# Kernel optimization log

Measured on AMD Instinct MI355X. Metric: run time of the kernel, lower is better.

Reference implementation:

```python
import jax, jax.numpy as jnp
import numpy as np

N_NODES = 100_000
N_EDGES = 1_600_000
IN_DIM = 512
HID = 128
OUT_DIM = 40


def setup_inputs() -> dict:
    key = jax.random.key(0)
    ks = jax.random.split(key, 12)
    s = 0.05  # small init scale
    x = jax.random.normal(ks[0], (N_NODES, IN_DIM), dtype=jnp.float32)
    edge_index = jax.random.randint(ks[1], (2, N_EDGES), 0, N_NODES, dtype=jnp.int64)
    W1 = jax.random.normal(ks[2], (IN_DIM, HID), dtype=jnp.float32) * s
    b1 = jnp.zeros((HID,), jnp.float32)
    Wg0 = jax.random.normal(ks[3], (HID, HID), dtype=jnp.float32) * s
    bg0 = jnp.zeros((HID,), jnp.float32)
    Wg1 = jax.random.normal(ks[4], (HID, HID), dtype=jnp.float32) * s
    bg1 = jnp.zeros((HID,), jnp.float32)
    W2 = jax.random.normal(ks[5], (HID, OUT_DIM), dtype=jnp.float32) * s
    b2 = jnp.zeros((OUT_DIM,), jnp.float32)
    return dict(x=x, edge_index=edge_index, W1=W1, b1=b1, Wg0=Wg0, bg0=bg0,
                Wg1=Wg1, bg1=bg1, W2=W2, b2=b2)


def _gcn_norm(edge_index, num_nodes, dtype):
    # PyG GCNConv default: add self-loops, symmetric normalization D^-1/2 A D^-1/2.
    loops = jnp.arange(num_nodes, dtype=edge_index.dtype)
    src = jnp.concatenate([edge_index[0], loops])  # [E+N]
    dst = jnp.concatenate([edge_index[1], loops])
    deg = jax.ops.segment_sum(jnp.ones(dst.shape, dtype), dst, num_segments=num_nodes)
    dinv = jnp.where(deg > 0, jax.lax.rsqrt(deg), jnp.zeros((), dtype))
    norm = dinv[src] * dinv[dst]  # [E+N]
    return src, dst, norm


def _gcn_conv(h, src, dst, norm, W, b, num_nodes):
    # out[dst] += norm * (h @ W)[src]; then bias
    hw = h @ W                              # [N, HID]
    msg = hw[src] * norm[:, None]           # gather + scale  [E+N, HID]
    agg = jax.ops.segment_sum(msg, dst, num_segments=num_nodes)  # scatter-add
    return agg + b


def reference(x, edge_index, W1, b1, Wg0, bg0, Wg1, bg1, W2, b2):
    n = x.shape[0]
    src, dst, norm = _gcn_norm(edge_index, n, x.dtype)
    h = jax.nn.relu(x @ W1 + b1)  # dropout is identity in eval mode
    for W, b in ((Wg0, bg0), (Wg1, bg1)):
        h = jax.nn.relu(_gcn_conv(h, src, dst, norm, W, b, n))
    logits = h @ W2 + b2
    return jax.nn.log_softmax(logits, axis=1)
```

## Files before the change

### kernel.cpp

```cpp
#include <hip/hip_runtime.h>
#include <hip/hip_bf16.h>
#include <cstdint>

#define HID 128

typedef short s16x8 __attribute__((ext_vector_type(8)));
typedef float f32x4 __attribute__((ext_vector_type(4)));

static inline size_t align_up(size_t x, size_t a) { return (x + a - 1) & ~(a - 1); }

__device__ inline ushort f2bf(float f) {
  uint u = __float_as_uint(f);
  u += 0x7FFFu + ((u >> 16) & 1u);
  return (ushort)(u >> 16);
}
__device__ inline float bf2f_lo(uint v) { return __uint_as_float(v << 16); }
__device__ inline float bf2f_hi(uint v) { return __uint_as_float(v & 0xFFFF0000u); }

__global__ void detect_i64_kernel(const unsigned int* __restrict__ p, int nwords,
                                  int* __restrict__ flag) {
  __shared__ int any;
  if (threadIdx.x == 0) any = 0;
  __syncthreads();
  for (int i = threadIdx.x; i < 1024; i += blockDim.x) {
    int w = 2 * i + 1;
    if (w < nwords && p[w] != 0u) atomicOr(&any, 1);
  }
  __syncthreads();
  if (threadIdx.x == 0) *flag = (any == 0) ? 1 : 0;
}

__global__ void extract_kernel(const void* __restrict__ ei, const int* __restrict__ flag,
                               int E, int* __restrict__ src32, int* __restrict__ dst32) {
  int e = blockIdx.x * blockDim.x + threadIdx.x;
  if (e >= E) return;
  if (*flag) {
    const long long* p = (const long long*)ei;
    src32[e] = (int)p[e];
    dst32[e] = (int)p[(size_t)E + e];
  } else {
    const int* p = (const int*)ei;
    src32[e] = p[e];
    dst32[e] = p[(size_t)E + e];
  }
}

__global__ void count_kernel(const int* __restrict__ dst32, int* __restrict__ cnt, int E) {
  int e = blockIdx.x * blockDim.x + threadIdx.x;
  if (e >= E) return;
  atomicAdd(&cnt[dst32[e]], 1);
}

__global__ void dinv_kernel(const int* __restrict__ cnt, float* __restrict__ dinv, int N) {
  int i = blockIdx.x * blockDim.x + threadIdx.x;
  if (i >= N) return;
  dinv[i] = rsqrtf((float)(cnt[i] + 1));
}

__global__ __launch_bounds__(1024) void scan_local_kernel(const int* __restrict__ cnt,
    int* __restrict__ off, int* __restrict__ bsum, int N) {
  __shared__ int buf[1024];
  int tid = threadIdx.x;
  int i = blockIdx.x * 1024 + tid;
  int v = (i < N) ? cnt[i] : 0;
  buf[tid] = v;
  __syncthreads();
  #pragma unroll
  for (int s = 1; s < 1024; s <<= 1) {
    int t = (tid >= s) ? buf[tid - s] : 0;
    __syncthreads();
    buf[tid] += t;
    __syncthreads();
  }
  if (i < N) off[i] = buf[tid] - v;
  if (tid == 1023) bsum[blockIdx.x] = buf[1023];
}

__global__ __launch_bounds__(128) void scan_bsum_kernel(const int* __restrict__ bsum, int nb,
    int* __restrict__ boff, int* __restrict__ offN) {
  __shared__ int b[128];
  int tid = threadIdx.x;
  int v = (tid < nb) ? bsum[tid] : 0;
  b[tid] = v;
  __syncthreads();
  #pragma unroll
  for (int s = 1; s < 128; s <<= 1) {
    int t = (tid >= s) ? b[tid - s] : 0;
    __syncthreads();
    b[tid] += t;
    __syncthreads();
  }
  if (tid < nb) boff[tid] = b[tid] - v;
  if (tid == 127) *offN = b[127];
}

__global__ void scan_add_kernel(int* __restrict__ off, const int* __restrict__ boff,
                                int* __restrict__ cursor, int N) {
  int i = blockIdx.x * blockDim.x + threadIdx.x;
  if (i >= N) return;
  int o = off[i] + boff[i >> 10];
  off[i] = o;
  cursor[i] = o;
}

__global__ void fill_kernel(const int* __restrict__ src32, const int* __restrict__ dst32,
                            const float* __restrict__ dinv, int* __restrict__ cursor,
                            int* __restrict__ csr_src, float* __restrict__ csr_norm, int E) {
  int e = blockIdx.x * blockDim.x + threadIdx.x;
  if (e >= E) return;
  int s = src32[e];
  int d = dst32[e];
  int pos = atomicAdd(&cursor[d], 1);
  csr_src[pos] = s;
  csr_norm[pos] = dinv[s] * dinv[d];
}

__global__ void convert_w_kernel(const float* __restrict__ W, ushort* __restrict__ Wt,
                                 int K, int KP) {
  int id = blockIdx.x * blockDim.x + threadIdx.x;
  if (id >= K * 128) return;
  int c = id & 127;
  int k = id >> 7;
  Wt[(size_t)c * KP + k] = f2bf(W[id]);
}

__global__ void convert_w2_kernel(const float* __restrict__ W2, ushort* __restrict__ Wt) {
  int id = blockIdx.x * blockDim.x + threadIdx.x;
  if (id >= 48 * 128) return;
  int c = id >> 7;
  int k = id & 127;
  Wt[(size_t)c * 128 + k] = (c < 40) ? f2bf(W2[(size_t)k * 40 + c]) : (ushort)0;
}

template <int K, bool AF32, bool BIAS_RELU, int WAVES>
__global__ __launch_bounds__(WAVES * 64, 16 / WAVES) void gemm_lds_kernel(
    const void* __restrict__ Ap, const ushort* __restrict__ Wtp,
    const float* __restrict__ bias, ushort* __restrict__ outp,
    int M, int rowsPerBlock) {
  constexpr int KP = K + 8;
  extern __shared__ __align__(16) ushort lB[];
  const int tid = threadIdx.x;

  const int rowStart = blockIdx.x * rowsPerBlock;
  if (rowStart >= M) return;
  const int rowEnd = min(M, rowStart + rowsPerBlock);

  constexpr int TOTC = 128 * KP / 8;
  const s16x8* Wt8 = (const s16x8*)Wtp;
  for (int i = tid; i < TOTC; i += WAVES * 64) ((s16x8*)lB)[i] = Wt8[i];
  __syncthreads();

  const int w = tid >> 6;
  const int l = tid & 63;
  const int l15 = l & 15;
  const int kg = l >> 4;

  const ushort* Ab = (const ushort*)Ap;
  const float* Af = (const float*)Ap;

  for (int base = rowStart + w * 16; base < rowEnd; base += WAVES * 16) {
    int row = base + l15;
    if (row >= M) row = M - 1;

    f32x4 acc[8];
    #pragma unroll
    for (int c = 0; c < 8; ++c) acc[c] = f32x4{0.f, 0.f, 0.f, 0.f};

    #pragma unroll 4
    for (int k0 = 0; k0 < K; k0 += 32) {
      s16x8 af;
      if constexpr (AF32) {
        const float* s = &Af[(size_t)row * K + k0 + kg * 8];
        float4 v0 = *(const float4*)s;
        float4 v1 = *(const float4*)(s + 4);
        af[0] = (short)f2bf(v0.x); af[1] = (short)f2bf(v0.y);
        af[2] = (short)f2bf(v0.z); af[3] = (short)f2bf(v0.w);
        af[4] = (short)f2bf(v1.x); af[5] = (short)f2bf(v1.y);
        af[6] = (short)f2bf(v1.z); af[7] = (short)f2bf(v1.w);
      } else {
        af = *(const s16x8*)&Ab[(size_t)row * K + k0 + kg * 8];
      }
      #pragma unroll
      for (int c = 0; c < 8; ++c) {
        s16x8 bfr = *(const s16x8*)&lB[(16 * c + l15) * KP + k0 + kg * 8];
        acc[c] = __builtin_amdgcn_mfma_f32_16x16x32_bf16(af, bfr, acc[c], 0, 0, 0);
      }
    }

    #pragma unroll
    for (int c = 0; c < 8; ++c) {
      float b = 0.f;
      if constexpr (BIAS_RELU) b = bias[16 * c + l15];
      #pragma unroll
      for (int v = 0; v < 4; ++v) {
        int r = base + kg * 4 + v;
        if (r < M) {
          float val = acc[c][v];
          if constexpr (BIAS_RELU) val = fmaxf(val + b, 0.f);
          outp[(size_t)r * 128 + 16 * c + l15] = f2bf(val);
        }
      }
    }
  }
}

__global__ __launch_bounds__(256) void aggregate_bf16_kernel(const ushort* __restrict__ hw,
    const int* __restrict__ off, const int* __restrict__ csr_src,
    const float* __restrict__ csr_norm, const float* __restrict__ dinv,
    const float* __restrict__ bias, ushort* __restrict__ out, int N) {
  int wid = (blockIdx.x * blockDim.x + threadIdx.x) >> 6;
  int lane = threadIdx.x & 63;
  if (wid >= N) return;
  const uint* hw4 = (const uint*)hw;
  int beg = off[wid], end = off[wid + 1];
  float ax = 0.f, ay = 0.f;
  int j = beg;
  for (; j + 4 <= end; j += 4) {
    int s0 = csr_src[j];
    int s1 = csr_src[j + 1];
    int s2 = csr_src[j + 2];
    int s3 = csr_src[j + 3];
    float n0 = csr_norm[j];
    float n1 = csr_norm[j + 1];
    float n2 = csr_norm[j + 2];
    float n3 = csr_norm[j + 3];
    uint v0 = hw4[(size_t)s0 * 64 + lane];
    uint v1 = hw4[(size_t)s1 * 64 + lane];
    uint v2 = hw4[(size_t)s2 * 64 + lane];
    uint v3 = hw4[(size_t)s3 * 64 + lane];
    ax = fmaf(n0, bf2f_lo(v0), ax); ay = fmaf(n0, bf2f_hi(v0), ay);
    ax = fmaf(n1, bf2f_lo(v1), ax); ay = fmaf(n1, bf2f_hi(v1), ay);
    ax = fmaf(n2, bf2f_lo(v2), ax); ay = fmaf(n2, bf2f_hi(v2), ay);
    ax = fmaf(n3, bf2f_lo(v3), ax); ay = fmaf(n3, bf2f_hi(v3), ay);
  }
  for (; j < end; ++j) {
    int s = csr_src[j];
    float nm = csr_norm[j];
    uint v = hw4[(size_t)s * 64 + lane];
    ax = fmaf(nm, bf2f_lo(v), ax);
    ay = fmaf(nm, bf2f_hi(v), ay);
  }
  float di = dinv[wid];
  float snm = di * di;
  uint v = hw4[(size_t)wid * 64 + lane];
  ax = fmaf(snm, bf2f_lo(v), ax);
  ay = fmaf(snm, bf2f_hi(v), ay);
  float2 b = ((const float2*)bias)[lane];
  float ox = fmaxf(ax + b.x, 0.f);
  float oy = fmaxf(ay + b.y, 0.f);
  ((uint*)out)[(size_t)wid * 64 + lane] = (uint)f2bf(ox) | ((uint)f2bf(oy) << 16);
}

__global__ __launch_bounds__(256) void final_mfma_kernel(const ushort* __restrict__ h,
    const ushort* __restrict__ W2t, const float* __restrict__ b2,
    float* __restrict__ out, int M) {
  const int tid = threadIdx.x;
  const int w = tid >> 6;
  const int l = tid & 63;
  const int l15 = l & 15;
  const int kg = l >> 4;
  const int base = (blockIdx.x * 4 + w) * 16;
  if (base >= M) return;
  int row = base + l15;
  if (row >= M) row = M - 1;

  f32x4 acc[3];
  #pragma unroll
  for (int c = 0; c < 3; ++c) acc[c] = f32x4{0.f, 0.f, 0.f, 0.f};

  #pragma unroll
  for (int k0 = 0; k0 < 128; k0 += 32) {
    s16x8 af = *(const s16x8*)&h[(size_t)row * 128 + k0 + kg * 8];
    #pragma unroll
    for (int c = 0; c < 3; ++c) {
      s16x8 bfr = *(const s16x8*)&W2t[(size_t)(16 * c + l15) * 128 + k0 + kg * 8];
      acc[c] = __builtin_amdgcn_mfma_f32_16x16x32_bf16(af, bfr, acc[c], 0, 0, 0);
    }
  }

  float bv0 = b2[l15];
  float bv1 = b2[16 + l15];
  float bv2 = (l15 < 8) ? b2[32 + l15] : 0.f;

  #pragma unroll
  for (int v = 0; v < 4; ++v) {
    float l0 = acc[0][v] + bv0;
    float l1 = acc[1][v] + bv1;
    float l2 = (l15 < 8) ? (acc[2][v] + bv2) : -1e30f;
    float pm = fmaxf(fmaxf(l0, l1), l2);
    #pragma unroll
    for (int sh = 8; sh > 0; sh >>= 1) pm = fmaxf(pm, __shfl_xor(pm, sh));
    float es = expf(l0 - pm) + expf(l1 - pm) + ((l15 < 8) ? expf(l2 - pm) : 0.f);
    #pragma unroll
    for (int sh = 8; sh > 0; sh >>= 1) es += __shfl_xor(es, sh);
    float lse = pm + logf(es);
    int r = base + kg * 4 + v;
    if (r < M) {
      out[(size_t)r * 40 + l15] = l0 - lse;
      out[(size_t)r * 40 + 16 + l15] = l1 - lse;
      if (l15 < 8) out[(size_t)r * 40 + 32 + l15] = l2 - lse;
    }
  }
}

extern "C" void kernel_launch(void* const* d_in, const int* in_sizes, int n_in,
                              void* d_out, int out_size, void* d_ws, size_t ws_size,
                              hipStream_t stream) {
  const float* x   = (const float*)d_in[0];
  const void*  ei  = d_in[1];
  const float* W1  = (const float*)d_in[2];
  const float* b1  = (const float*)d_in[3];
  const float* Wg0 = (const float*)d_in[4];
  const float* bg0 = (const float*)d_in[5];
  const float* Wg1 = (const float*)d_in[6];
  const float* bg1 = (const float*)d_in[7];
  const float* W2  = (const float*)d_in[8];
  const float* b2  = (const float*)d_in[9];
  float* out = (float*)d_out;

  const int N = in_sizes[0] / 512;
  const int E = in_sizes[1] / 2;

  char* wsb = (char*)d_ws;
  size_t o = 0;
  auto alloc = [&](size_t bytes) -> void* {
    void* p = wsb + o;
    o = align_up(o + bytes, 256);
    return p;
  };
  int*    flag    = (int*)alloc(4);
  int*    src32   = (int*)alloc((size_t)E * 4);
  int*    dst32   = (int*)alloc((size_t)E * 4);
  int*    cnt     = (int*)alloc((size_t)N * 4);
  float*  dinv    = (float*)alloc((size_t)N * 4);
  int*    off     = (int*)alloc((size_t)(N + 1) * 4);
  int*    cursor  = (int*)alloc((size_t)N * 4);
  int*    bsum    = (int*)alloc(128 * 4);
  int*    boff    = (int*)alloc(128 * 4);
  int*    csr_src = (int*)alloc((size_t)E * 4);
  float*  csr_nrm = (float*)alloc((size_t)E * 4);
  ushort* W1t     = (ushort*)alloc((size_t)128 * 520 * 2);
  ushort* Wg0t    = (ushort*)alloc((size_t)128 * 136 * 2);
  ushort* Wg1t    = (ushort*)alloc((size_t)128 * 136 * 2);
  ushort* W2t     = (ushort*)alloc((size_t)48 * 128 * 2);
  ushort* hb1     = (ushort*)alloc((size_t)N * HID * 2);
  ushort* hb2     = (ushort*)alloc((size_t)N * HID * 2);
  (void)ws_size; (void)n_in; (void)out_size;

  const int tpb = 256;
  const int ebl = (E + tpb - 1) / tpb;
  const int nbl = (N + tpb - 1) / tpb;

  detect_i64_kernel<<<1, 256, 0, stream>>>((const unsigned int*)ei, 2 * E, flag);
  extract_kernel<<<ebl, tpb, 0, stream>>>(ei, flag, E, src32, dst32);
  hipMemsetAsync(cnt, 0, (size_t)N * 4, stream);
  count_kernel<<<ebl, tpb, 0, stream>>>(dst32, cnt, E);
  dinv_kernel<<<nbl, tpb, 0, stream>>>(cnt, dinv, N);
  const int nsb = (N + 1023) / 1024;
  scan_local_kernel<<<nsb, 1024, 0, stream>>>(cnt, off, bsum, N);
  scan_bsum_kernel<<<1, 128, 0, stream>>>(bsum, nsb, boff, off + N);
  scan_add_kernel<<<nbl, tpb, 0, stream>>>(off, boff, cursor, N);
  fill_kernel<<<ebl, tpb, 0, stream>>>(src32, dst32, dinv, cursor, csr_src, csr_nrm, E);

  convert_w_kernel<<<(512 * 128 + 255) / 256, 256, 0, stream>>>(W1, W1t, 512, 520);
  convert_w_kernel<<<(128 * 128 + 255) / 256, 256, 0, stream>>>(Wg0, Wg0t, 128, 136);
  convert_w_kernel<<<(128 * 128 + 255) / 256, 256, 0, stream>>>(Wg1, Wg1t, 128, 136);
  convert_w2_kernel<<<(48 * 128 + 255) / 256, 256, 0, stream>>>(W2, W2t);

  const size_t lds512 = (size_t)128 * 520 * 2;
  const size_t lds128 = (size_t)128 * 136 * 2;
  static bool attr_done = false;
  if (!attr_done) {
    (void)hipFuncSetAttribute(
        reinterpret_cast<const void*>(&gemm_lds_kernel<512, true, true, 8>),
        hipFuncAttributeMaxDynamicSharedMemorySize, (int)lds512);
    attr_done = true;
  }

  int rpb512 = (N + 255) / 256;
  rpb512 = (rpb512 + 15) & ~15;
  const int grid512 = (N + rpb512 - 1) / rpb512;
  const int rpb128 = 128;
  const int grid128 = (N + rpb128 - 1) / rpb128;
  const int abl = (N * 64 + tpb - 1) / tpb;
  const int fbl = (N + 63) / 64;

  gemm_lds_kernel<512, true, true, 8><<<grid512, 512, lds512, stream>>>(
      x, W1t, b1, hb1, N, rpb512);

  gemm_lds_kernel<128, false, false, 4><<<grid128, 256, lds128, stream>>>(
      hb1, Wg0t, nullptr, hb2, N, rpb128);
  aggregate_bf16_kernel<<<abl, tpb, 0, stream>>>(hb2, off, csr_src, csr_nrm, dinv, bg0, hb1, N);

  gemm_lds_kernel<128, false, false, 4><<<grid128, 256, lds128, stream>>>(
      hb1, Wg1t, nullptr, hb2, N, rpb128);
  aggregate_bf16_kernel<<<abl, tpb, 0, stream>>>(hb2, off, csr_src, csr_nrm, dinv, bg1, hb1, N);

  final_mfma_kernel<<<fbl, 256, 0, stream>>>(hb1, W2t, b2, out, N);
}
```

Before: 490.9 us.

## Fuse edge extract with degree count, pack bf16 conversions, widen first GEMM blocks

Merges the edge-index extraction and degree-count kernels into one launch, so dst32 no longer has to be re-read from memory. Replaces the scalar bf16 rounding with a packed float2-to-bf162 intrinsic in the first GEMM's A-load path and in the aggregate output store. Raises the 512-K input GEMM from 8 to 16 waves per block (1024 threads), giving each LDS-resident copy of W1 twice as many waves to share it. The larger block may increase register pressure under the new launch bound.

Result: no change. 481.9 us (-1.8%).

```diff
diff --git a/kernel.cpp b/kernel.cpp
--- a/kernel.cpp
+++ b/kernel.cpp
@@ -13,6 +13,10 @@
   uint u = __float_as_uint(f);
   u += 0x7FFFu + ((u >> 16) & 1u);
   return (ushort)(u >> 16);
+}
+__device__ inline uint pk2bf(float lo, float hi) {
+  __hip_bfloat162 h = __float22bfloat162_rn(float2{lo, hi});
+  return *reinterpret_cast<uint*>(&h);
 }
 __device__ inline float bf2f_lo(uint v) { return __uint_as_float(v << 16); }
 __device__ inline float bf2f_hi(uint v) { return __uint_as_float(v & 0xFFFF0000u); }
@@ -30,25 +34,24 @@
   if (threadIdx.x == 0) *flag = (any == 0) ? 1 : 0;
 }
 
-__global__ void extract_kernel(const void* __restrict__ ei, const int* __restrict__ flag,
-                               int E, int* __restrict__ src32, int* __restrict__ dst32) {
+__global__ void extract_count_kernel(const void* __restrict__ ei, const int* __restrict__ flag,
+                                     int E, int* __restrict__ src32, int* __restrict__ dst32,
+                                     int* __restrict__ cnt) {
   int e = blockIdx.x * blockDim.x + threadIdx.x;
   if (e >= E) return;
+  int s, d;
   if (*flag) {
     const long long* p = (const long long*)ei;
-    src32[e] = (int)p[e];
-    dst32[e] = (int)p[(size_t)E + e];
+    s = (int)p[e];
+    d = (int)p[(size_t)E + e];
   } else {
     const int* p = (const int*)ei;
-    src32[e] = p[e];
-    dst32[e] = p[(size_t)E + e];
-  }
-}
-
-__global__ void count_kernel(const int* __restrict__ dst32, int* __restrict__ cnt, int E) {
-  int e = blockIdx.x * blockDim.x + threadIdx.x;
-  if (e >= E) return;
-  atomicAdd(&cnt[dst32[e]], 1);
+    s = p[e];
+    d = p[(size_t)E + e];
+  }
+  src32[e] = s;
+  dst32[e] = d;
+  atomicAdd(&cnt[d], 1);
 }
 
 __global__ void dinv_kernel(const int* __restrict__ cnt, float* __restrict__ dinv, int N) {
@@ -133,7 +136,8 @@
 }
 
 template <int K, bool AF32, bool BIAS_RELU, int WAVES>
-__global__ __launch_bounds__(WAVES * 64, 16 / WAVES) void gemm_lds_kernel(
+__global__ __launch_bounds__(WAVES * 64, (WAVES == 16) ? 4 : 16 / WAVES)
+void gemm_lds_kernel(
     const void* __restrict__ Ap, const ushort* __restrict__ Wtp,
     const float* __restrict__ bias, ushort* __restrict__ outp,
     int M, int rowsPerBlock) {
@@ -173,10 +177,12 @@
         const float* s = &Af[(size_t)row * K + k0 + kg * 8];
         float4 v0 = *(const float4*)s;
         float4 v1 = *(const float4*)(s + 4);
-        af[0] = (short)f2bf(v0.x); af[1] = (short)f2bf(v0.y);
-        af[2] = (short)f2bf(v0.z); af[3] = (short)f2bf(v0.w);
-        af[4] = (short)f2bf(v1.x); af[5] = (short)f2bf(v1.y);
-        af[6] = (short)f2bf(v1.z); af[7] = (short)f2bf(v1.w);
+        uint4 u;
+        u.x = pk2bf(v0.x, v0.y);
+        u.y = pk2bf(v0.z, v0.w);
+        u.z = pk2bf(v1.x, v1.y);
+        u.w = pk2bf(v1.z, v1.w);
+        af = *reinterpret_cast<s16x8*>(&u);
       } else {
         af = *(const s16x8*)&Ab[(size_t)row * K + k0 + kg * 8];
       }
@@ -248,7 +254,7 @@
   float2 b = ((const float2*)bias)[lane];
   float ox = fmaxf(ax + b.x, 0.f);
   float oy = fmaxf(ay + b.y, 0.f);
-  ((uint*)out)[(size_t)wid * 64 + lane] = (uint)f2bf(ox) | ((uint)f2bf(oy) << 16);
+  ((uint*)out)[(size_t)wid * 64 + lane] = pk2bf(ox, oy);
 }
 
 __global__ __launch_bounds__(256) void final_mfma_kernel(const ushort* __restrict__ h,
@@ -352,9 +358,8 @@
   const int nbl = (N + tpb - 1) / tpb;
 
   detect_i64_kernel<<<1, 256, 0, stream>>>((const unsigned int*)ei, 2 * E, flag);
-  extract_kernel<<<ebl, tpb, 0, stream>>>(ei, flag, E, src32, dst32);
   hipMemsetAsync(cnt, 0, (size_t)N * 4, stream);
-  count_kernel<<<ebl, tpb, 0, stream>>>(dst32, cnt, E);
+  extract_count_kernel<<<ebl, tpb, 0, stream>>>(ei, flag, E, src32, dst32, cnt);
   dinv_kernel<<<nbl, tpb, 0, stream>>>(cnt, dinv, N);
   const int nsb = (N + 1023) / 1024;
   scan_local_kernel<<<nsb, 1024, 0, stream>>>(cnt, off, bsum, N);
@@ -372,7 +377,7 @@
   static bool attr_done = false;
   if (!attr_done) {
     (void)hipFuncSetAttribute(
-        reinterpret_cast<const void*>(&gemm_lds_kernel<512, true, true, 8>),
+        reinterpret_cast<const void*>(&gemm_lds_kernel<512, true, true, 16>),
         hipFuncAttributeMaxDynamicSharedMemorySize, (int)lds512);
     attr_done = true;
   }
@@ -385,7 +390,7 @@
   const int abl = (N * 64 + tpb - 1) / tpb;
   const int fbl = (N + 63) / 64;
 
-  gemm_lds_kernel<512, true, true, 8><<<grid512, 512, lds512, stream>>>(
+  gemm_lds_kernel<512, true, true, 16><<<grid512, 1024, lds512, stream>>>(
       x, W1t, b1, hb1, N, rpb512);
 
   gemm_lds_kernel<128, false, false, 4><<<grid128, 256, lds128, stream>>>(
```
